# Optimization experiments

Hardware: AMD Instinct MI355X
Metric: run time of the kernel (lower is better)

The kernel has to match this reference:

```python
import jax, jax.numpy as jnp
import numpy as np
from jax import lax

EPS = 1e-5

def binarize_ste(x):
    # sign binarization to {-1,+1} (0 -> +1) with straight-through gradient
    s = jnp.where(x >= 0, 1.0, -1.0).astype(x.dtype)
    return x + lax.stop_gradient(s - x)

def bn(x, gamma, beta, mean, var):
    # inference-mode batchnorm; broadcast over channel axis 1 for 4D, axis 1 for 2D
    if x.ndim == 4:
        shape = (1, -1, 1, 1)
    else:
        shape = (1, -1)
    inv = gamma.reshape(shape) / jnp.sqrt(var.reshape(shape) + EPS)
    return (x - mean.reshape(shape)) * inv + beta.reshape(shape)

def conv_rep(x, w):
    # replicate (edge) padding of 1, then valid 3x3 conv, NCHW/OIHW
    xp = jnp.pad(x, ((0, 0), (0, 0), (1, 1), (1, 1)), mode='edge')
    return lax.conv_general_dilated(xp, binarize_ste(w), (1, 1), 'VALID',
                                    dimension_numbers=('NCHW', 'OIHW', 'NCHW'))

def maxpool2(x):
    return lax.reduce_window(x, -jnp.inf, lax.max, (1, 1, 2, 2), (1, 1, 2, 2), 'VALID')

def hardtanh(x):
    return jnp.clip(x, -1.0, 1.0)

def setup_inputs() -> dict:
    key = jax.random.key(0)
    ks = jax.random.split(key, 16)
    B = 2048
    inp = {
        'x': jax.random.normal(ks[0], (B, 1, 28, 28), jnp.float32),
        'conv1_w': jax.random.normal(ks[1], (64, 1, 3, 3), jnp.float32),
        'bn1_gamma': jax.random.uniform(ks[2], (64,), jnp.float32),
        'bn1_beta': jax.random.normal(ks[3], (64,), jnp.float32),
        'bn1_mean': jax.random.normal(ks[4], (64,), jnp.float32),
        'bn1_var': jax.random.uniform(ks[5], (64,), jnp.float32),
        'conv2_w': jax.random.normal(ks[6], (64, 64, 3, 3), jnp.float32),
        'bn2_gamma': jax.random.uniform(ks[7], (64,), jnp.float32),
        'bn2_beta': jax.random.normal(ks[8], (64,), jnp.float32),
        'bn2_mean': jax.random.normal(ks[9], (64,), jnp.float32),
        'bn2_var': jax.random.uniform(ks[10], (64,), jnp.float32),
        'fc1_w': jax.random.normal(ks[11], (2048, 3136), jnp.float32),
        'bn3_gamma': jax.random.uniform(ks[12], (2048,), jnp.float32),
        'bn3_beta': jax.random.normal(ks[13], (2048,), jnp.float32),
        'bn3_mean': jax.random.normal(ks[14], (2048,), jnp.float32),
        'bn3_var': jax.random.uniform(ks[15], (2048,), jnp.float32),
        'fc2_w': jax.random.normal(jax.random.fold_in(key, 99), (10, 2048), jnp.float32),
        'scale': jnp.array([0.001], jnp.float32),
    }
    return inp

def reference(x, conv1_w, bn1_gamma, bn1_beta, bn1_mean, bn1_var,
              conv2_w, bn2_gamma, bn2_beta, bn2_mean, bn2_var,
              fc1_w, bn3_gamma, bn3_beta, bn3_mean, bn3_var,
              fc2_w, scale):
    # block 1: binarized conv -> BN -> hardtanh -> binarize -> maxpool
    h = conv_rep(x, conv1_w)                          # [B,64,28,28]
    h = binarize_ste(hardtanh(bn(h, bn1_gamma, bn1_beta, bn1_mean, bn1_var)))
    h = maxpool2(h)                                   # [B,64,14,14]
    # block 2
    h = conv_rep(h, conv2_w)                          # [B,64,14,14]
    h = binarize_ste(hardtanh(bn(h, bn2_gamma, bn2_beta, bn2_mean, bn2_var)))
    h = maxpool2(h)                                   # [B,64,7,7]
    h = h.reshape(h.shape[0], -1)                     # [B,3136] (C*H*W order)
    # fc block
    h = h @ binarize_ste(fc1_w).T                     # [B,2048]
    h = binarize_ste(hardtanh(bn(h, bn3_gamma, bn3_beta, bn3_mean, bn3_var)))
    h = h @ binarize_ste(fc2_w).T                     # [B,10]
    return h * scale
```

## Files before the change

### kernel.cpp

```cpp
#include <hip/hip_runtime.h>
#include <cstdint>

#define EPS 1e-5f

typedef unsigned long long u64;
typedef unsigned short u16;

__device__ __forceinline__ int clampi(int v, int lo, int hi) {
    return v < lo ? lo : (v > hi ? hi : v);
}


__global__ void prep_conv1(const float* __restrict__ w, float* __restrict__ s1) {
    int t = blockIdx.x * blockDim.x + threadIdx.x;
    if (t < 64 * 9) s1[t] = (w[t] >= 0.f) ? 1.f : -1.f;
}

__global__ void prep_conv2(const float* __restrict__ w, u64* __restrict__ w2p) {
    int t = blockIdx.x * blockDim.x + threadIdx.x;
    if (t >= 64 * 9) return;
    int co = t / 9, tap = t % 9;
    u64 word = 0;
    for (int ci = 0; ci < 64; ci++) {
        word |= (u64)(w[(co * 64 + ci) * 9 + tap] >= 0.f) << ci;
    }
    w2p[t] = word;
}

__global__ void prep_fc1(const float* __restrict__ w, u64* __restrict__ wp) {
    int o = blockIdx.x;
    int p = threadIdx.x;
    if (p >= 49) return;
    const float* row = w + o * 3136;
    u64 word = 0;
    for (int c = 0; c < 64; c++) {
        word |= (u64)(row[c * 49 + p] >= 0.f) << c;
    }
    wp[p * 2048 + o] = word;
}

__global__ void prep_fc2(const float* __restrict__ w, u64* __restrict__ w2) {
    int t = blockIdx.x * blockDim.x + threadIdx.x;
    if (t >= 10 * 32) return;
    int o = t / 32, k = t % 32;
    u64 word = 0;
    for (int j = 0; j < 64; j++) {
        word |= (u64)(w[o * 2048 + k * 64 + j] >= 0.f) << j;
    }
    w2[t] = word;
}


__global__ __launch_bounds__(256) void k_conv1(
    const float* __restrict__ x, const float* __restrict__ s1,
    const float* __restrict__ g_, const float* __restrict__ bt,
    const float* __restrict__ mn, const float* __restrict__ vr,
    u64* __restrict__ out1)
{
    __shared__ float sw[144];
    __shared__ float sm[16], si[16], sb[16];
    int tid = threadIdx.x;
    int g = blockIdx.y;
    int base = g * 16;
    if (tid < 144) sw[tid] = s1[base * 9 + tid];
    if (tid < 16) {
        si[tid] = g_[base + tid] / sqrtf(vr[base + tid] + EPS);
        sm[tid] = mn[base + tid];
        sb[tid] = bt[base + tid];
    }
    __syncthreads();

    int idx = blockIdx.x * 256 + tid;
    int b = idx / 196, p = idx % 196;
    int pi = p / 14, pj = p % 14;

    float patch[4][4];
    const float* xb = x + b * 784;
    for (int r = 0; r < 4; r++) {
        int rr = clampi(2 * pi - 1 + r, 0, 27);
        for (int c = 0; c < 4; c++) {
            int cc = clampi(2 * pj - 1 + c, 0, 27);
            patch[r][c] = xb[rr * 28 + cc];
        }
    }

    unsigned word = 0;
    for (int ch = 0; ch < 16; ch++) {
        const float* w = &sw[ch * 9];
        float m = sm[ch], iv = si[ch], be = sb[ch];
        int bit = 0;
        #pragma unroll
        for (int di = 0; di < 2; di++)
        #pragma unroll
        for (int dj = 0; dj < 2; dj++) {
            float v = 0.f;
            #pragma unroll
            for (int ki = 0; ki < 3; ki++)
            #pragma unroll
            for (int kj = 0; kj < 3; kj++)
                v += patch[di + ki][dj + kj] * w[ki * 3 + kj];
            float y = (v - m) * iv + be;
            bit |= (y >= 0.f);
        }
        word |= (unsigned)bit << ch;
    }
    ((u16*)out1)[idx * 4 + g] = (u16)word;
}


__global__ __launch_bounds__(256) void k_conv2(
    const u64* __restrict__ in, const u64* __restrict__ w2p,
    const float* __restrict__ g_, const float* __restrict__ bt,
    const float* __restrict__ mn, const float* __restrict__ vr,
    u64* __restrict__ out2)
{
    __shared__ u64 sw[144];
    __shared__ float sm[16], si[16], sb[16];
    int tid = threadIdx.x;
    int g = blockIdx.y;
    int base = g * 16;
    if (tid < 144) sw[tid] = w2p[base * 9 + tid];
    if (tid < 16) {
        si[tid] = g_[base + tid] / sqrtf(vr[base + tid] + EPS);
        sm[tid] = mn[base + tid];
        sb[tid] = bt[base + tid];
    }
    __syncthreads();

    int idx = blockIdx.x * 256 + tid;
    int b = idx / 49, p = idx % 49;
    int pi = p / 7, pj = p % 7;

    u64 a[4][4];
    const u64* ib = in + b * 196;
    for (int r = 0; r < 4; r++) {
        int rr = clampi(2 * pi - 1 + r, 0, 13);
        for (int c = 0; c < 4; c++) {
            int cc = clampi(2 * pj - 1 + c, 0, 13);
            a[r][c] = ib[rr * 14 + cc];
        }
    }

    unsigned word = 0;
    for (int co = 0; co < 16; co++) {
        const u64* w = &sw[co * 9];
        int s00 = 0, s01 = 0, s10 = 0, s11 = 0;
        #pragma unroll
        for (int ki = 0; ki < 3; ki++)
        #pragma unroll
        for (int kj = 0; kj < 3; kj++) {
            u64 ww = w[ki * 3 + kj];
            s00 += __popcll(a[ki][kj] ^ ww);
            s01 += __popcll(a[ki][kj + 1] ^ ww);
            s10 += __popcll(a[ki + 1][kj] ^ ww);
            s11 += __popcll(a[ki + 1][kj + 1] ^ ww);
        }
        int smin = min(min(s00, s01), min(s10, s11));
        int smax = max(max(s00, s01), max(s10, s11));
        float m = sm[co], iv = si[co], be = sb[co];
        int bit = (((float)(576 - 2 * smin) - m) * iv + be >= 0.f) |
                  (((float)(576 - 2 * smax) - m) * iv + be >= 0.f);
        word |= (unsigned)bit << co;
    }
    ((u16*)out2)[idx * 4 + g] = (u16)word;
}


#define NB 8

__global__ __launch_bounds__(256) void k_fc1(
    const u64* __restrict__ act, const u64* __restrict__ wp,
    const float* __restrict__ g, const float* __restrict__ bt,
    const float* __restrict__ mn, const float* __restrict__ vr,
    u64* __restrict__ out3)
{
    __shared__ u64 sa[NB * 49];
    int tid = threadIdx.x;
    int btile = blockIdx.x >> 3;
    int otile = blockIdx.x & 7;
    int b0 = btile * NB;
    int o = otile * 256 + tid;

    for (int i = tid; i < NB * 49; i += 256) {
        int bb = i / 49, p = i % 49;
        sa[i] = act[(b0 + bb) * 49 + p];
    }
    __syncthreads();

    int sums[NB];
    #pragma unroll
    for (int i = 0; i < NB; i++) sums[i] = 0;

    for (int p = 0; p < 49; p++) {
        u64 w = wp[p * 2048 + o];
        #pragma unroll
        for (int bb = 0; bb < NB; bb++)
            sums[bb] += __popcll(sa[bb * 49 + p] ^ w);
    }

    float iv = g[o] / sqrtf(vr[o] + EPS);
    float m = mn[o], be = bt[o];
    #pragma unroll
    for (int bb = 0; bb < NB; bb++) {
        float y = ((float)(3136 - 2 * sums[bb]) - m) * iv + be;
        u64 ball = __ballot(y >= 0.f);
        if ((tid & 63) == 0) out3[(b0 + bb) * 32 + (o >> 6)] = ball;
    }
}


__global__ void k_fc2(const u64* __restrict__ act, const u64* __restrict__ w2,
                      const float* __restrict__ scale, float* __restrict__ out)
{
    int idx = blockIdx.x * 256 + threadIdx.x;
    if (idx >= 2048 * 16) return;
    int b = idx >> 4, o = idx & 15;
    if (o >= 10) return;
    int s = 0;
    #pragma unroll
    for (int k = 0; k < 32; k++)
        s += __popcll(act[b * 32 + k] ^ w2[o * 32 + k]);
    out[b * 10 + o] = scale[0] * (float)(2048 - 2 * s);
}


extern "C" void kernel_launch(void* const* d_in, const int* in_sizes, int n_in,
                              void* d_out, int out_size, void* d_ws, size_t ws_size,
                              hipStream_t stream) {
    const float* x        = (const float*)d_in[0];
    const float* conv1_w  = (const float*)d_in[1];
    const float* bn1_g    = (const float*)d_in[2];
    const float* bn1_b    = (const float*)d_in[3];
    const float* bn1_m    = (const float*)d_in[4];
    const float* bn1_v    = (const float*)d_in[5];
    const float* conv2_w  = (const float*)d_in[6];
    const float* bn2_g    = (const float*)d_in[7];
    const float* bn2_b    = (const float*)d_in[8];
    const float* bn2_m    = (const float*)d_in[9];
    const float* bn2_v    = (const float*)d_in[10];
    const float* fc1_w    = (const float*)d_in[11];
    const float* bn3_g    = (const float*)d_in[12];
    const float* bn3_b    = (const float*)d_in[13];
    const float* bn3_m    = (const float*)d_in[14];
    const float* bn3_v    = (const float*)d_in[15];
    const float* fc2_w    = (const float*)d_in[16];
    const float* scale    = (const float*)d_in[17];
    float* out = (float*)d_out;

    char* ws = (char*)d_ws;
    float* s1   = (float*)(ws + 0);
    u64*   w2p  = (u64*)  (ws + 2560);
    u64*   wp   = (u64*)  (ws + 8192);
    u64*   w2pk = (u64*)  (ws + 811008);
    u64*   out1 = (u64*)  (ws + 813568);
    u64*   out2 = (u64*)  (ws + 4024832);
    u64*   out3 = (u64*)  (ws + 4827648);

    hipLaunchKernelGGL(prep_conv1, dim3(3), dim3(256), 0, stream, conv1_w, s1);
    hipLaunchKernelGGL(prep_conv2, dim3(3), dim3(256), 0, stream, conv2_w, w2p);
    hipLaunchKernelGGL(prep_fc1, dim3(2048), dim3(64), 0, stream, fc1_w, wp);
    hipLaunchKernelGGL(prep_fc2, dim3(2), dim3(256), 0, stream, fc2_w, w2pk);

    hipLaunchKernelGGL(k_conv1, dim3(1568, 4), dim3(256), 0, stream,
                       x, s1, bn1_g, bn1_b, bn1_m, bn1_v, out1);
    hipLaunchKernelGGL(k_conv2, dim3(392, 4), dim3(256), 0, stream,
                       out1, w2p, bn2_g, bn2_b, bn2_m, bn2_v, out2);
    hipLaunchKernelGGL(k_fc1, dim3(2048), dim3(256), 0, stream,
                       out2, wp, bn3_g, bn3_b, bn3_m, bn3_v, out3);
    hipLaunchKernelGGL(k_fc2, dim3(128), dim3(256), 0, stream,
                       out3, w2pk, scale, out);
}
```

Before: 230.1 us.

## Merge small prep kernels, precompute BN constants, and stage fc1 rows in LDS

Merges the three small weight-packing kernels and the BN constant computation into one prep launch, which cuts launch count and per-block sqrt/divide work. prep_fc1 now loads each fc1 row into shared memory with float4 reads so the strided bit-packing reads come from LDS rather than global memory. conv1 now evaluates only min/max of the 2x2 pooled window through BN, matching what conv2 already does, and both conv kernels read weights directly from global memory instead of staging them in shared memory. fc1 batch tile is doubled to reuse each weight load across more samples, halving the grid.

Result: faster. 212.6 us (-7.6%).

```diff
diff --git a/kernel.cpp b/kernel.cpp
--- a/kernel.cpp
+++ b/kernel.cpp
@@ -11,97 +11,107 @@
 }
 
 
-__global__ void prep_conv1(const float* __restrict__ w, float* __restrict__ s1) {
-    int t = blockIdx.x * blockDim.x + threadIdx.x;
-    if (t < 64 * 9) s1[t] = (w[t] >= 0.f) ? 1.f : -1.f;
-}
-
-__global__ void prep_conv2(const float* __restrict__ w, u64* __restrict__ w2p) {
-    int t = blockIdx.x * blockDim.x + threadIdx.x;
-    if (t >= 64 * 9) return;
-    int co = t / 9, tap = t % 9;
-    u64 word = 0;
-    for (int ci = 0; ci < 64; ci++) {
-        word |= (u64)(w[(co * 64 + ci) * 9 + tap] >= 0.f) << ci;
-    }
-    w2p[t] = word;
-}
-
-__global__ void prep_fc1(const float* __restrict__ w, u64* __restrict__ wp) {
+__global__ void prep_small(
+    const float* __restrict__ conv1_w, const float* __restrict__ conv2_w,
+    const float* __restrict__ fc2_w,
+    const float* __restrict__ g1, const float* __restrict__ b1,
+    const float* __restrict__ m1, const float* __restrict__ v1,
+    const float* __restrict__ g2, const float* __restrict__ b2,
+    const float* __restrict__ m2, const float* __restrict__ v2,
+    float* __restrict__ s1, u64* __restrict__ w2p, u64* __restrict__ w2pk,
+    float4* __restrict__ bnc1, float4* __restrict__ bnc2)
+{
+    int t = blockIdx.x * 256 + threadIdx.x;
+    if (t < 576) {
+        s1[t] = (conv1_w[t] >= 0.f) ? 1.f : -1.f;
+    } else if (t < 1152) {
+        int u = t - 576;
+        int co = u / 9, tap = u % 9;
+        u64 word = 0;
+        for (int ci = 0; ci < 64; ci++)
+            word |= (u64)(conv2_w[(co * 64 + ci) * 9 + tap] >= 0.f) << ci;
+        w2p[u] = word;
+    } else if (t < 1472) {
+        int u = t - 1152;
+        int o = u / 32, k = u % 32;
+        u64 word = 0;
+        for (int j = 0; j < 64; j++)
+            word |= (u64)(fc2_w[o * 2048 + k * 64 + j] >= 0.f) << j;
+        w2pk[u] = word;
+    } else if (t < 1536) {
+        int ch = t - 1472;
+        bnc1[ch] = make_float4(m1[ch], g1[ch] / sqrtf(v1[ch] + EPS), b1[ch], 0.f);
+    } else if (t < 1600) {
+        int ch = t - 1536;
+        bnc2[ch] = make_float4(m2[ch], g2[ch] / sqrtf(v2[ch] + EPS), b2[ch], 0.f);
+    }
+}
+
+
+__global__ __launch_bounds__(256) void prep_fc1(const float* __restrict__ w,
+                                                u64* __restrict__ wp) {
+    __shared__ float ls[3136];
     int o = blockIdx.x;
+    const float4* row4 = (const float4*)(w + o * 3136);
+    for (int i = threadIdx.x; i < 784; i += 256)
+        ((float4*)ls)[i] = row4[i];
+    __syncthreads();
     int p = threadIdx.x;
-    if (p >= 49) return;
-    const float* row = w + o * 3136;
-    u64 word = 0;
-    for (int c = 0; c < 64; c++) {
-        word |= (u64)(row[c * 49 + p] >= 0.f) << c;
-    }
-    wp[p * 2048 + o] = word;
-}
-
-__global__ void prep_fc2(const float* __restrict__ w, u64* __restrict__ w2) {
-    int t = blockIdx.x * blockDim.x + threadIdx.x;
-    if (t >= 10 * 32) return;
-    int o = t / 32, k = t % 32;
-    u64 word = 0;
-    for (int j = 0; j < 64; j++) {
-        word |= (u64)(w[o * 2048 + k * 64 + j] >= 0.f) << j;
-    }
-    w2[t] = word;
+    if (p < 49) {
+        u64 word = 0;
+        #pragma unroll
+        for (int c = 0; c < 64; c++)
+            word |= (u64)(ls[c * 49 + p] >= 0.f) << c;
+        wp[p * 2048 + o] = word;
+    }
 }
 
 
 __global__ __launch_bounds__(256) void k_conv1(
     const float* __restrict__ x, const float* __restrict__ s1,
-    const float* __restrict__ g_, const float* __restrict__ bt,
-    const float* __restrict__ mn, const float* __restrict__ vr,
-    u64* __restrict__ out1)
-{
-    __shared__ float sw[144];
-    __shared__ float sm[16], si[16], sb[16];
+    const float4* __restrict__ bnc1, u64* __restrict__ out1)
+{
     int tid = threadIdx.x;
     int g = blockIdx.y;
     int base = g * 16;
-    if (tid < 144) sw[tid] = s1[base * 9 + tid];
-    if (tid < 16) {
-        si[tid] = g_[base + tid] / sqrtf(vr[base + tid] + EPS);
-        sm[tid] = mn[base + tid];
-        sb[tid] = bt[base + tid];
-    }
-    __syncthreads();
 
     int idx = blockIdx.x * 256 + tid;
     int b = idx / 196, p = idx % 196;
     int pi = p / 14, pj = p % 14;
 
+    const float* xb = x + b * 784;
+    int rr[4], cc[4];
+    #pragma unroll
+    for (int r = 0; r < 4; r++) rr[r] = clampi(2 * pi - 1 + r, 0, 27) * 28;
+    #pragma unroll
+    for (int c = 0; c < 4; c++) cc[c] = clampi(2 * pj - 1 + c, 0, 27);
     float patch[4][4];
-    const float* xb = x + b * 784;
-    for (int r = 0; r < 4; r++) {
-        int rr = clampi(2 * pi - 1 + r, 0, 27);
-        for (int c = 0; c < 4; c++) {
-            int cc = clampi(2 * pj - 1 + c, 0, 27);
-            patch[r][c] = xb[rr * 28 + cc];
-        }
-    }
+    #pragma unroll
+    for (int r = 0; r < 4; r++)
+        #pragma unroll
+        for (int c = 0; c < 4; c++)
+            patch[r][c] = xb[rr[r] + cc[c]];
 
     unsigned word = 0;
+    #pragma unroll 4
     for (int ch = 0; ch < 16; ch++) {
-        const float* w = &sw[ch * 9];
-        float m = sm[ch], iv = si[ch], be = sb[ch];
-        int bit = 0;
-        #pragma unroll
-        for (int di = 0; di < 2; di++)
-        #pragma unroll
-        for (int dj = 0; dj < 2; dj++) {
-            float v = 0.f;
+        const float* w = s1 + (base + ch) * 9;
+        float v00 = 0.f, v01 = 0.f, v10 = 0.f, v11 = 0.f;
+        #pragma unroll
+        for (int ki = 0; ki < 3; ki++)
             #pragma unroll
-            for (int ki = 0; ki < 3; ki++)
-            #pragma unroll
-            for (int kj = 0; kj < 3; kj++)
-                v += patch[di + ki][dj + kj] * w[ki * 3 + kj];
-            float y = (v - m) * iv + be;
-            bit |= (y >= 0.f);
-        }
+            for (int kj = 0; kj < 3; kj++) {
+                float ww = w[ki * 3 + kj];
+                v00 += patch[ki][kj] * ww;
+                v01 += patch[ki][kj + 1] * ww;
+                v10 += patch[ki + 1][kj] * ww;
+                v11 += patch[ki + 1][kj + 1] * ww;
+            }
+        float vmin = fminf(fminf(v00, v01), fminf(v10, v11));
+        float vmax = fmaxf(fmaxf(v00, v01), fmaxf(v10, v11));
+        float4 c4 = bnc1[base + ch];
+        int bit = (((vmin - c4.x) * c4.y + c4.z) >= 0.f) |
+                  (((vmax - c4.x) * c4.y + c4.z) >= 0.f);
         word |= (unsigned)bit << ch;
     }
     ((u16*)out1)[idx * 4 + g] = (u16)word;
@@ -110,63 +120,56 @@
 
 __global__ __launch_bounds__(256) void k_conv2(
     const u64* __restrict__ in, const u64* __restrict__ w2p,
-    const float* __restrict__ g_, const float* __restrict__ bt,
-    const float* __restrict__ mn, const float* __restrict__ vr,
-    u64* __restrict__ out2)
-{
-    __shared__ u64 sw[144];
-    __shared__ float sm[16], si[16], sb[16];
+    const float4* __restrict__ bnc2, u64* __restrict__ out2)
+{
     int tid = threadIdx.x;
     int g = blockIdx.y;
     int base = g * 16;
-    if (tid < 144) sw[tid] = w2p[base * 9 + tid];
-    if (tid < 16) {
-        si[tid] = g_[base + tid] / sqrtf(vr[base + tid] + EPS);
-        sm[tid] = mn[base + tid];
-        sb[tid] = bt[base + tid];
-    }
-    __syncthreads();
 
     int idx = blockIdx.x * 256 + tid;
     int b = idx / 49, p = idx % 49;
     int pi = p / 7, pj = p % 7;
 
+    const u64* ib = in + b * 196;
+    int rr[4], cc[4];
+    #pragma unroll
+    for (int r = 0; r < 4; r++) rr[r] = clampi(2 * pi - 1 + r, 0, 13) * 14;
+    #pragma unroll
+    for (int c = 0; c < 4; c++) cc[c] = clampi(2 * pj - 1 + c, 0, 13);
     u64 a[4][4];
-    const u64* ib = in + b * 196;
-    for (int r = 0; r < 4; r++) {
-        int rr = clampi(2 * pi - 1 + r, 0, 13);
-        for (int c = 0; c < 4; c++) {
-            int cc = clampi(2 * pj - 1 + c, 0, 13);
-            a[r][c] = ib[rr * 14 + cc];
-        }
-    }
+    #pragma unroll
+    for (int r = 0; r < 4; r++)
+        #pragma unroll
+        for (int c = 0; c < 4; c++)
+            a[r][c] = ib[rr[r] + cc[c]];
 
     unsigned word = 0;
+    #pragma unroll 2
     for (int co = 0; co < 16; co++) {
-        const u64* w = &sw[co * 9];
+        const u64* w = w2p + (base + co) * 9;
         int s00 = 0, s01 = 0, s10 = 0, s11 = 0;
         #pragma unroll
         for (int ki = 0; ki < 3; ki++)
-        #pragma unroll
-        for (int kj = 0; kj < 3; kj++) {
-            u64 ww = w[ki * 3 + kj];
-            s00 += __popcll(a[ki][kj] ^ ww);
-            s01 += __popcll(a[ki][kj + 1] ^ ww);
-            s10 += __popcll(a[ki + 1][kj] ^ ww);
-            s11 += __popcll(a[ki + 1][kj + 1] ^ ww);
-        }
+            #pragma unroll
+            for (int kj = 0; kj < 3; kj++) {
+                u64 ww = w[ki * 3 + kj];
+                s00 += __popcll(a[ki][kj] ^ ww);
+                s01 += __popcll(a[ki][kj + 1] ^ ww);
+                s10 += __popcll(a[ki + 1][kj] ^ ww);
+                s11 += __popcll(a[ki + 1][kj + 1] ^ ww);
+            }
         int smin = min(min(s00, s01), min(s10, s11));
         int smax = max(max(s00, s01), max(s10, s11));
-        float m = sm[co], iv = si[co], be = sb[co];
-        int bit = (((float)(576 - 2 * smin) - m) * iv + be >= 0.f) |
-                  (((float)(576 - 2 * smax) - m) * iv + be >= 0.f);
+        float4 c4 = bnc2[base + co];
+        int bit = (((float)(576 - 2 * smin) - c4.x) * c4.y + c4.z >= 0.f) |
+                  (((float)(576 - 2 * smax) - c4.x) * c4.y + c4.z >= 0.f);
         word |= (unsigned)bit << co;
     }
     ((u16*)out2)[idx * 4 + g] = (u16)word;
 }
 
 
-#define NB 8
+#define NB 16
 
 __global__ __launch_bounds__(256) void k_fc1(
     const u64* __restrict__ act, const u64* __restrict__ wp,
@@ -248,24 +251,28 @@
     float* out = (float*)d_out;
 
     char* ws = (char*)d_ws;
-    float* s1   = (float*)(ws + 0);
-    u64*   w2p  = (u64*)  (ws + 2560);
-    u64*   wp   = (u64*)  (ws + 8192);
-    u64*   w2pk = (u64*)  (ws + 811008);
-    u64*   out1 = (u64*)  (ws + 813568);
-    u64*   out2 = (u64*)  (ws + 4024832);
-    u64*   out3 = (u64*)  (ws + 4827648);
-
-    hipLaunchKernelGGL(prep_conv1, dim3(3), dim3(256), 0, stream, conv1_w, s1);
-    hipLaunchKernelGGL(prep_conv2, dim3(3), dim3(256), 0, stream, conv2_w, w2p);
-    hipLaunchKernelGGL(prep_fc1, dim3(2048), dim3(64), 0, stream, fc1_w, wp);
-    hipLaunchKernelGGL(prep_fc2, dim3(2), dim3(256), 0, stream, fc2_w, w2pk);
+    float*  s1   = (float*) (ws + 0);
+    u64*    w2p  = (u64*)   (ws + 2560);
+    float4* bnc1 = (float4*)(ws + 7168);
+    u64*    wp   = (u64*)   (ws + 8192);
+    u64*    w2pk = (u64*)   (ws + 811008);
+    float4* bnc2 = (float4*)(ws + 813568);
+    u64*    out1 = (u64*)   (ws + 819200);
+    u64*    out2 = (u64*)   (ws + 4030464);
+    u64*    out3 = (u64*)   (ws + 4833280);
+
+    hipLaunchKernelGGL(prep_small, dim3(7), dim3(256), 0, stream,
+                       conv1_w, conv2_w, fc2_w,
+                       bn1_g, bn1_b, bn1_m, bn1_v,
+                       bn2_g, bn2_b, bn2_m, bn2_v,
+                       s1, w2p, w2pk, bnc1, bnc2);
+    hipLaunchKernelGGL(prep_fc1, dim3(2048), dim3(256), 0, stream, fc1_w, wp);
 
     hipLaunchKernelGGL(k_conv1, dim3(1568, 4), dim3(256), 0, stream,
-                       x, s1, bn1_g, bn1_b, bn1_m, bn1_v, out1);
+                       x, s1, bnc1, out1);
     hipLaunchKernelGGL(k_conv2, dim3(392, 4), dim3(256), 0, stream,
-                       out1, w2p, bn2_g, bn2_b, bn2_m, bn2_v, out2);
-    hipLaunchKernelGGL(k_fc1, dim3(2048), dim3(256), 0, stream,
+                       out1, w2p, bnc2, out2);
+    hipLaunchKernelGGL(k_fc1, dim3(1024), dim3(256), 0, stream,
                        out2, wp, bn3_g, bn3_b, bn3_m, bn3_v, out3);
     hipLaunchKernelGGL(k_fc2, dim3(128), dim3(256), 0, stream,
                        out3, w2pk, scale, out);
```
